# Kernel tuning notes

Hardware: AMD Instinct MI355X
Metric: run time of the kernel (lower is better)

Reference implementation:

```python
import jax, jax.numpy as jnp
import numpy as np
import math

DIM = 768
NUM_HEADS = 12
HEAD_DIM = DIM // NUM_HEADS


def setup_inputs() -> dict:
    key = jax.random.key(0)
    k_x, k_q, k_k, k_v = jax.random.split(key, 4)
    s = 1.0 / math.sqrt(DIM)
    return {
        "x": jax.random.normal(k_x, (2, 2048, DIM), dtype=jnp.float32),
        "Wq": jax.random.normal(k_q, (DIM, DIM), dtype=jnp.float32) * s,
        "Wk": jax.random.normal(k_k, (DIM, DIM), dtype=jnp.float32) * s,
        "Wv": jax.random.normal(k_v, (DIM, DIM), dtype=jnp.float32) * s,
    }


def reference(x, Wq, Wk, Wv):
    b, n, _ = x.shape
    # nn.Linear(dim, dim, bias=False): y = x @ W.T
    def split_heads(y):
        return y.reshape(b, n, NUM_HEADS, HEAD_DIM).transpose(0, 2, 1, 3)  # b h n d
    Q = split_heads(x @ Wq.T)
    K = split_heads(x @ Wk.T)
    V = split_heads(x @ Wv.T)
    scores = jnp.einsum('bhqd,bhkd->bhqk', Q, K)
    # FAITHFUL to source: softmax over the HEADS axis (dim=1), then scale by 1/sqrt(dim)
    attn = jax.nn.softmax(scores, axis=1) / math.sqrt(DIM)
    out = jnp.einsum('bhqk,bhkd->bhqd', attn, V)
    out = out.transpose(0, 2, 1, 3).reshape(b, n, DIM)  # b n (h d)
    return out  # to_out is Identity (project_out=False)
```

## Files before the change

### kernel.cpp

```cpp
#include <hip/hip_runtime.h>

#define DIM 768
#define NHEADS 12
#define HDIM 64
#define BATCH 2
#define SEQ 2048
#define ROWS (BATCH*SEQ)
#define KSPLIT 4

typedef __attribute__((ext_vector_type(8))) _Float16 f16x8;
typedef __attribute__((ext_vector_type(4))) _Float16 f16x4;
typedef __attribute__((ext_vector_type(2))) _Float16 f16x2;
typedef __attribute__((ext_vector_type(4))) float    f32x4;

__device__ __forceinline__ void dma16(const _Float16* g, _Float16* l) {
    __builtin_amdgcn_global_load_lds(
        (const __attribute__((address_space(1))) unsigned int*)g,
        (__attribute__((address_space(3))) unsigned int*)l, 16, 0, 0);
}


__global__ __launch_bounds__(256) void cvt_all(
    const float* __restrict__ x,  const float* __restrict__ wq,
    const float* __restrict__ wk, const float* __restrict__ wv,
    _Float16* __restrict__ xf,  _Float16* __restrict__ wqf,
    _Float16* __restrict__ wkf, _Float16* __restrict__ wvf)
{
    const int lane = threadIdx.x & 63;
    const int wid  = (blockIdx.x * 256 + threadIdx.x) >> 6;
    const float* src; _Float16* dst; int t;
    if (wid < 6144)      { src = x;  dst = xf;  t = wid;        }
    else if (wid < 7296) { src = wq; dst = wqf; t = wid - 6144; }
    else if (wid < 8448) { src = wk; dst = wkf; t = wid - 7296; }
    else                 { src = wv; dst = wvf; t = wid - 8448; }
    const int c = lane & 15, quad = lane >> 4;
    const int mt = t / 24, kt = t % 24;
    const float* p = src + (size_t)(mt*16 + c) * 768 + kt*32 + quad*8;
    float4 v0 = *(const float4*)p;
    float4 v1 = *(const float4*)(p + 4);
    f16x8 o;
    o[0]=(_Float16)v0.x; o[1]=(_Float16)v0.y; o[2]=(_Float16)v0.z; o[3]=(_Float16)v0.w;
    o[4]=(_Float16)v1.x; o[5]=(_Float16)v1.y; o[6]=(_Float16)v1.z; o[7]=(_Float16)v1.w;
    *reinterpret_cast<f16x8*>(dst + ((size_t)t * 64 + lane) * 8) = o;
}

__global__ __launch_bounds__(256) void gemm3(
    const _Float16* __restrict__ xf, const _Float16* __restrict__ wqkf,
    const _Float16* __restrict__ wvf,
    _Float16* __restrict__ Qf, _Float16* __restrict__ Kf, _Float16* __restrict__ Vkt)
{
    __shared__ _Float16 Ab[2][8*512];
    __shared__ _Float16 Bb[2][8*512];
    const int tid = threadIdx.x, lane = tid & 63, w = tid >> 6;
    const int c = lane & 15, quad = lane >> 4;

    const _Float16 *Af, *Bf;
    int mt0, nt0, mode;
    if ((int)blockIdx.x < 384) {
        int mt = blockIdx.x / 12, nt = blockIdx.x % 12;
        Af = xf; Bf = wqkf; mt0 = mt*8; nt0 = nt*8; mode = 0;
    } else {
        int v = blockIdx.x - 384;
        int mt = v / 32, nt = v % 32;
        Af = wvf; Bf = xf; mt0 = mt*8; nt0 = nt*8; mode = 1;
    }

    auto stage = [&](int kt, int buf) {
#pragma unroll
        for (int u = 0; u < 4; ++u) {
            const int cc = w*4 + u;
            const _Float16* s = (cc < 8) ? Af + ((size_t)(mt0+cc)*24 + kt)*512
                                         : Bf + ((size_t)(nt0+cc-8)*24 + kt)*512;
            _Float16* d = (cc < 8) ? &Ab[buf][cc*512] : &Bb[buf][(cc-8)*512];
            dma16(s + lane*8, d);
        }
    };

    stage(0, 0);
    __syncthreads();

    f32x4 acc[4][4] = {};
    for (int kt = 0; kt < 24; ++kt) {
        const int cur = kt & 1;
        if (kt < 23) stage(kt+1, cur^1);
        f16x8 a[4], b[4];
#pragma unroll
        for (int i = 0; i < 4; ++i)
            a[i] = *(const f16x8*)(&Ab[cur][((w>>1)*4 + i)*512] + lane*8);
#pragma unroll
        for (int j = 0; j < 4; ++j)
            b[j] = *(const f16x8*)(&Bb[cur][((w&1)*4 + j)*512] + lane*8);
#pragma unroll
        for (int i = 0; i < 4; ++i)
#pragma unroll
            for (int j = 0; j < 4; ++j)
                acc[i][j] = __builtin_amdgcn_mfma_f32_16x16x32_f16(a[i], b[j], acc[i][j], 0,0,0);
        __syncthreads();
    }

    _Float16* L = &Ab[0][0] + w*1280;
#pragma unroll
    for (int i2 = 0; i2 < 2; ++i2)
#pragma unroll
        for (int j2 = 0; j2 < 2; ++j2) {
#pragma unroll
            for (int ii = 0; ii < 2; ++ii)
#pragma unroll
                for (int jj = 0; jj < 2; ++jj)
#pragma unroll
                    for (int r = 0; r < 4; ++r)
                        L[(ii*16 + quad*4 + r)*40 + jj*16 + c] =
                            (_Float16)acc[i2*2+ii][j2*2+jj][r];
#pragma unroll
            for (int ii = 0; ii < 2; ++ii) {
                const int mtg = mt0 + (w>>1)*4 + i2*2 + ii;
                if (mode == 0) {
                    f16x8 v = *(const f16x8*)(L + (ii*16 + c)*40 + quad*8);
                    const int nt32 = (nt0 + (w&1)*4)/2 + j2;
                    _Float16* dst = (nt32 < 24)
                        ? Qf + ((size_t)(mtg*24 + nt32)*64 + lane)*8
                        : Kf + ((size_t)(mtg*24 + nt32 - 24)*64 + lane)*8;
                    *(f16x8*)dst = v;
                } else {
#pragma unroll
                    for (int jj = 0; jj < 2; ++jj) {
                        f16x4 v4 = *(const f16x4*)(L + (ii*16 + c)*40 + jj*16 + quad*4);
                        const int kcu = nt0 + (w&1)*4 + j2*2 + jj;
                        *(f16x4*)(Vkt + ((size_t)kcu*48 + mtg)*256 + lane*4) = v4;
                    }
                }
            }
        }
}

__global__ __launch_bounds__(1024) __attribute__((amdgpu_waves_per_eu(4)))
void attn_kernel(
    const _Float16* __restrict__ Qf, const _Float16* __restrict__ Kf,
    const _Float16* __restrict__ Vkt,
    float* __restrict__ out,
    _Float16* __restrict__ part)
{
    __shared__ __attribute__((aligned(16))) _Float16 Kb[24*512];
    __shared__ __attribute__((aligned(16))) float    Ps[16][16][20];
    __shared__ __attribute__((aligned(16))) _Float16 Pl[4][12][16][20];
    const int tid = threadIdx.x, lane = tid & 63, w = tid >> 6;
    const int c = lane & 15, quad = lane >> 4;
    const int qi = w >> 2, g = w & 3;

    const int bid = blockIdx.x;
    const int qb = bid & 31;
    const int ks = (bid >> 5) & 3;
    const int b  = bid >> 7;
    const int qrow0 = b*SEQ + qb*64;
    const int qt16  = (qrow0 >> 4) + qi;
    const int kb16  = (b*SEQ + ks*(SEQ/KSPLIT)) >> 4;

    f16x8 qreg[6];
#pragma unroll
    for (int u = 0; u < 6; ++u)
        qreg[u] = *(const f16x8*)(Qf + ((size_t)(qt16*24 + g*6 + u)*64 + lane)*8);

    const _Float16* Vb0 = Vkt + ((size_t)kb16*48 + g)*256 + lane*4;

    if (w < 12) {
#pragma unroll
        for (int u = 0; u < 2; ++u)
            dma16(Kf + ((size_t)kb16*24 + w*2 + u)*512 + lane*8, &Kb[(w*2+u)*512]);
    }
    __syncthreads();

    f32x4 o_acc[12] = {};
    f16x4 vv[12];
    f32x4 e3[3];

    for (int t = 0; t < 32; ++t) {
#pragma unroll
        for (int hh = 0; hh < 3; ++hh) {
            f16x8 ka = *(const f16x8*)(&Kb[(g*6 + hh*2    )*512] + lane*8);
            f16x8 k2 = *(const f16x8*)(&Kb[(g*6 + hh*2 + 1)*512] + lane*8);
            f32x4 a = {};
            a = __builtin_amdgcn_mfma_f32_16x16x32_f16(ka, qreg[hh*2],   a, 0,0,0);
            a = __builtin_amdgcn_mfma_f32_16x16x32_f16(k2, qreg[hh*2+1], a, 0,0,0);
            f32x4 ee;
#pragma unroll
            for (int r = 0; r < 4; ++r) ee[r] = __expf(a[r]);
            e3[hh] = ee;
        }
        {
            f32x4 ps;
#pragma unroll
            for (int r = 0; r < 4; ++r) ps[r] = e3[0][r] + e3[1][r] + e3[2][r];
            *(f32x4*)&Ps[qi*4+g][c][quad*4] = ps;
        }
        if (t > 0) {
#pragma unroll
            for (int h = 6; h < 12; ++h)
                vv[h] = *(const f16x4*)(Vb0 + ((size_t)(t-1)*48 + h*4)*256);
#pragma unroll
            for (int h = 0; h < 12; ++h) {
                f16x4 pf = *(const f16x4*)&Pl[qi][h][c][quad*4];
                o_acc[h] = __builtin_amdgcn_mfma_f32_16x16x16f16(vv[h], pf, o_acc[h], 0,0,0);
            }
        }
        __syncthreads();
        if (w < 12 && t < 31) {
#pragma unroll
            for (int u = 0; u < 2; ++u)
                dma16(Kf + ((size_t)(kb16+t+1)*24 + w*2 + u)*512 + lane*8,
                      &Kb[(w*2+u)*512]);
        }
        {
            f32x4 s0 = *(const f32x4*)&Ps[qi*4+0][c][quad*4];
            f32x4 s1 = *(const f32x4*)&Ps[qi*4+1][c][quad*4];
            f32x4 s2 = *(const f32x4*)&Ps[qi*4+2][c][quad*4];
            f32x4 s3 = *(const f32x4*)&Ps[qi*4+3][c][quad*4];
            f32x4 inv;
#pragma unroll
            for (int r = 0; r < 4; ++r)
                inv[r] = 1.0f / ((s0[r]+s1[r]+s2[r]+s3[r]) * 27.712812921102035f);
#pragma unroll
            for (int hh = 0; hh < 3; ++hh) {
                f16x4 pw;
#pragma unroll
                for (int r = 0; r < 4; ++r) pw[r] = (_Float16)(e3[hh][r]*inv[r]);
                *(f16x4*)&Pl[qi][g*3+hh][c][quad*4] = pw;
            }
        }
#pragma unroll
        for (int h = 0; h < 6; ++h)
            vv[h] = *(const f16x4*)(Vb0 + ((size_t)t*48 + h*4)*256);
        __syncthreads();
    }
#pragma unroll
    for (int h = 6; h < 12; ++h)
        vv[h] = *(const f16x4*)(Vb0 + ((size_t)31*48 + h*4)*256);
#pragma unroll
    for (int h = 0; h < 12; ++h) {
        f16x4 pf = *(const f16x4*)&Pl[qi][h][c][quad*4];
        o_acc[h] = __builtin_amdgcn_mfma_f32_16x16x16f16(vv[h], pf, o_acc[h], 0,0,0);
    }

    if (ks == 0) {
#pragma unroll
        for (int h = 0; h < 12; ++h)
            *(f32x4*)(out + (size_t)(qrow0 + qi*16 + c)*DIM + h*64 + g*16 + quad*4)
                = o_acc[h];
    } else {
        _Float16* dst = part + (size_t)(ks - 1) * ROWS * DIM;
#pragma unroll
        for (int h = 0; h < 12; ++h) {
            f16x4 v;
#pragma unroll
            for (int r = 0; r < 4; ++r) v[r] = (_Float16)o_acc[h][r];
            *(f16x4*)(dst + (size_t)(qrow0 + qi*16 + c)*DIM + h*64 + g*16 + quad*4) = v;
        }
    }
}

__global__ __launch_bounds__(256) void reduce_add4(
    float* __restrict__ out, const _Float16* __restrict__ part, int n4)
{
    int i = blockIdx.x * 256 + threadIdx.x;
    if (i >= n4) return;
    float4 o = reinterpret_cast<float4*>(out)[i];
    const size_t N = (size_t)ROWS * DIM;
#pragma unroll
    for (int p = 0; p < 3; ++p) {
        f16x4 v = reinterpret_cast<const f16x4*>(part + p * N)[i];
        o.x += (float)v[0]; o.y += (float)v[1]; o.z += (float)v[2]; o.w += (float)v[3];
    }
    reinterpret_cast<float4*>(out)[i] = o;
}

extern "C" void kernel_launch(void* const* d_in, const int* in_sizes, int n_in,
                              void* d_out, int out_size, void* d_ws, size_t ws_size,
                              hipStream_t stream)
{
    const float* x  = (const float*)d_in[0];
    const float* Wq = (const float*)d_in[1];
    const float* Wk = (const float*)d_in[2];
    const float* Wv = (const float*)d_in[3];

    _Float16* ws  = (_Float16*)d_ws;
    const size_t XS = (size_t)ROWS * DIM;
    const size_t WS = (size_t)DIM * DIM;
    _Float16* xf   = ws;
    _Float16* wqf  = xf  + XS;
    _Float16* wkf  = wqf + WS;
    _Float16* wvf  = wkf + WS;
    _Float16* Qf   = wvf + WS;
    _Float16* Kf   = Qf  + XS;
    _Float16* Vkt  = Kf  + XS;
    _Float16* part = Vkt + XS;

    cvt_all<<<2400, 256, 0, stream>>>(x, Wq, Wk, Wv, xf, wqf, wkf, wvf);
    gemm3<<<576, 256, 0, stream>>>(xf, wqf, wvf, Qf, Kf, Vkt);
    attn_kernel<<<BATCH * KSPLIT * 32, 1024, 0, stream>>>(
        Qf, Kf, Vkt, (float*)d_out, part);
    reduce_add4<<<(int)(XS/4 + 255)/256, 256, 0, stream>>>(
        (float*)d_out, part, (int)(XS/4));
}
```

Before: 188.6 us.

## Prefetch K tiles through registers and use LDS-only barriers

Replaces the global_load_lds DMA of K tiles with register prefetch two steps ahead, storing into LDS after the barrier. __syncthreads is replaced with s_waitcnt lgkmcnt(0) plus s_barrier, so outstanding global loads (V and K prefetch) no longer block at barriers. All 12 V fragments are now loaded at the end of each step rather than split across two phases, and the Ps scratch layout changes to a padded flat layout meant to reduce LDS bank conflicts. This raises register pressure and relies on the compiler inserting vmcnt waits correctly before the prefetched registers are used.

Result: slower. 230.7 us (+22.3%).

```diff
diff --git a/kernel.cpp b/kernel.cpp
--- a/kernel.cpp
+++ b/kernel.cpp
@@ -17,6 +17,10 @@
     __builtin_amdgcn_global_load_lds(
         (const __attribute__((address_space(1))) unsigned int*)g,
         (__attribute__((address_space(3))) unsigned int*)l, 16, 0, 0);
+}
+
+__device__ __forceinline__ void barrier_lgkm() {
+    asm volatile("s_waitcnt lgkmcnt(0)\n\ts_barrier" ::: "memory");
 }
 
 
@@ -141,7 +145,7 @@
     _Float16* __restrict__ part)
 {
     __shared__ __attribute__((aligned(16))) _Float16 Kb[24*512];
-    __shared__ __attribute__((aligned(16))) float    Ps[16][16][20];
+    __shared__ __attribute__((aligned(16))) float    Ps[16][336];
     __shared__ __attribute__((aligned(16))) _Float16 Pl[4][12][16][20];
     const int tid = threadIdx.x, lane = tid & 63, w = tid >> 6;
     const int c = lane & 15, quad = lane >> 4;
@@ -154,6 +158,7 @@
     const int qrow0 = b*SEQ + qb*64;
     const int qt16  = (qrow0 >> 4) + qi;
     const int kb16  = (b*SEQ + ks*(SEQ/KSPLIT)) >> 4;
+    const int psoff = quad*84 + c*4;
 
     f16x8 qreg[6];
 #pragma unroll
@@ -162,12 +167,17 @@
 
     const _Float16* Vb0 = Vkt + ((size_t)kb16*48 + g)*256 + lane*4;
 
+    f16x8 kreg0, kreg1;
     if (w < 12) {
-#pragma unroll
-        for (int u = 0; u < 2; ++u)
-            dma16(Kf + ((size_t)kb16*24 + w*2 + u)*512 + lane*8, &Kb[(w*2+u)*512]);
-    }
-    __syncthreads();
+        const _Float16* kp = Kf + ((size_t)kb16*24 + w*2)*512 + lane*8;
+        kreg0 = *(const f16x8*)(kp);
+        kreg1 = *(const f16x8*)(kp + 512);
+        *(f16x8*)(&Kb[(w*2+0)*512] + lane*8) = kreg0;
+        *(f16x8*)(&Kb[(w*2+1)*512] + lane*8) = kreg1;
+        kreg0 = *(const f16x8*)(kp + 24*512);
+        kreg1 = *(const f16x8*)(kp + 24*512 + 512);
+    }
+    barrier_lgkm();
 
     f32x4 o_acc[12] = {};
     f16x4 vv[12];
@@ -190,30 +200,30 @@
             f32x4 ps;
 #pragma unroll
             for (int r = 0; r < 4; ++r) ps[r] = e3[0][r] + e3[1][r] + e3[2][r];
-            *(f32x4*)&Ps[qi*4+g][c][quad*4] = ps;
+            *(f32x4*)&Ps[qi*4+g][psoff] = ps;
         }
         if (t > 0) {
-#pragma unroll
-            for (int h = 6; h < 12; ++h)
-                vv[h] = *(const f16x4*)(Vb0 + ((size_t)(t-1)*48 + h*4)*256);
 #pragma unroll
             for (int h = 0; h < 12; ++h) {
                 f16x4 pf = *(const f16x4*)&Pl[qi][h][c][quad*4];
                 o_acc[h] = __builtin_amdgcn_mfma_f32_16x16x16f16(vv[h], pf, o_acc[h], 0,0,0);
             }
         }
-        __syncthreads();
+        barrier_lgkm();
         if (w < 12 && t < 31) {
-#pragma unroll
-            for (int u = 0; u < 2; ++u)
-                dma16(Kf + ((size_t)(kb16+t+1)*24 + w*2 + u)*512 + lane*8,
-                      &Kb[(w*2+u)*512]);
+            *(f16x8*)(&Kb[(w*2+0)*512] + lane*8) = kreg0;
+            *(f16x8*)(&Kb[(w*2+1)*512] + lane*8) = kreg1;
+            if (t < 30) {
+                const _Float16* kp = Kf + ((size_t)(kb16+t+2)*24 + w*2)*512 + lane*8;
+                kreg0 = *(const f16x8*)(kp);
+                kreg1 = *(const f16x8*)(kp + 512);
+            }
         }
         {
-            f32x4 s0 = *(const f32x4*)&Ps[qi*4+0][c][quad*4];
-            f32x4 s1 = *(const f32x4*)&Ps[qi*4+1][c][quad*4];
-            f32x4 s2 = *(const f32x4*)&Ps[qi*4+2][c][quad*4];
-            f32x4 s3 = *(const f32x4*)&Ps[qi*4+3][c][quad*4];
+            f32x4 s0 = *(const f32x4*)&Ps[qi*4+0][psoff];
+            f32x4 s1 = *(const f32x4*)&Ps[qi*4+1][psoff];
+            f32x4 s2 = *(const f32x4*)&Ps[qi*4+2][psoff];
+            f32x4 s3 = *(const f32x4*)&Ps[qi*4+3][psoff];
             f32x4 inv;
 #pragma unroll
             for (int r = 0; r < 4; ++r)
@@ -227,13 +237,10 @@
             }
         }
 #pragma unroll
-        for (int h = 0; h < 6; ++h)
+        for (int h = 0; h < 12; ++h)
             vv[h] = *(const f16x4*)(Vb0 + ((size_t)t*48 + h*4)*256);
-        __syncthreads();
-    }
-#pragma unroll
-    for (int h = 6; h < 12; ++h)
-        vv[h] = *(const f16x4*)(Vb0 + ((size_t)31*48 + h*4)*256);
+        barrier_lgkm();
+    }
 #pragma unroll
     for (int h = 0; h < 12; ++h) {
         f16x4 pf = *(const f16x4*)&Pl[qi][h][c][quad*4];
```

## Halve attention block size, fold log2e into Wq, use exp2 and fast reciprocal

Applied to the files above, without the earlier changes.

Shrinks the attention block from 1024 to 512 threads, with 32 query rows per block and twice as many blocks. Every wave now issues three K DMA loads, where before only 12 of 16 waves issued two each. Wq is pre-scaled by log2(e) during conversion so the softmax can use the hardware exp2 instead of expf, and the normaliser uses a fast rcp instead of a divide. The Ps LDS layout is padded differently to reduce bank conflicts, and all 12 V loads are issued together after the barrier. Together these aim to raise occupancy and cut transcendental cost, but K is loaded twice as often overall and precision drops slightly.

Result: no change. 188.2 us (-0.2%).

```diff
diff --git a/kernel.cpp b/kernel.cpp
--- a/kernel.cpp
+++ b/kernel.cpp
@@ -29,8 +29,9 @@
     const int lane = threadIdx.x & 63;
     const int wid  = (blockIdx.x * 256 + threadIdx.x) >> 6;
     const float* src; _Float16* dst; int t;
+    float sc = 1.0f;
     if (wid < 6144)      { src = x;  dst = xf;  t = wid;        }
-    else if (wid < 7296) { src = wq; dst = wqf; t = wid - 6144; }
+    else if (wid < 7296) { src = wq; dst = wqf; t = wid - 6144; sc = 1.4426950408889634f; }
     else if (wid < 8448) { src = wk; dst = wkf; t = wid - 7296; }
     else                 { src = wv; dst = wvf; t = wid - 8448; }
     const int c = lane & 15, quad = lane >> 4;
@@ -39,8 +40,8 @@
     float4 v0 = *(const float4*)p;
     float4 v1 = *(const float4*)(p + 4);
     f16x8 o;
-    o[0]=(_Float16)v0.x; o[1]=(_Float16)v0.y; o[2]=(_Float16)v0.z; o[3]=(_Float16)v0.w;
-    o[4]=(_Float16)v1.x; o[5]=(_Float16)v1.y; o[6]=(_Float16)v1.z; o[7]=(_Float16)v1.w;
+    o[0]=(_Float16)(v0.x*sc); o[1]=(_Float16)(v0.y*sc); o[2]=(_Float16)(v0.z*sc); o[3]=(_Float16)(v0.w*sc);
+    o[4]=(_Float16)(v1.x*sc); o[5]=(_Float16)(v1.y*sc); o[6]=(_Float16)(v1.z*sc); o[7]=(_Float16)(v1.w*sc);
     *reinterpret_cast<f16x8*>(dst + ((size_t)t * 64 + lane) * 8) = o;
 }
 
@@ -133,7 +134,7 @@
         }
 }
 
-__global__ __launch_bounds__(1024) __attribute__((amdgpu_waves_per_eu(4)))
+__global__ __launch_bounds__(512) __attribute__((amdgpu_waves_per_eu(4)))
 void attn_kernel(
     const _Float16* __restrict__ Qf, const _Float16* __restrict__ Kf,
     const _Float16* __restrict__ Vkt,
@@ -141,19 +142,20 @@
     _Float16* __restrict__ part)
 {
     __shared__ __attribute__((aligned(16))) _Float16 Kb[24*512];
-    __shared__ __attribute__((aligned(16))) float    Ps[16][16][20];
-    __shared__ __attribute__((aligned(16))) _Float16 Pl[4][12][16][20];
+    __shared__ __attribute__((aligned(16))) float    Ps[8][336];
+    __shared__ __attribute__((aligned(16))) _Float16 Pl[2][12][16][20];
     const int tid = threadIdx.x, lane = tid & 63, w = tid >> 6;
     const int c = lane & 15, quad = lane >> 4;
     const int qi = w >> 2, g = w & 3;
 
     const int bid = blockIdx.x;
-    const int qb = bid & 31;
-    const int ks = (bid >> 5) & 3;
-    const int b  = bid >> 7;
-    const int qrow0 = b*SEQ + qb*64;
+    const int qb = bid & 63;
+    const int ks = (bid >> 6) & 3;
+    const int b  = bid >> 8;
+    const int qrow0 = b*SEQ + qb*32;
     const int qt16  = (qrow0 >> 4) + qi;
     const int kb16  = (b*SEQ + ks*(SEQ/KSPLIT)) >> 4;
+    const int psoff = quad*84 + c*4;
 
     f16x8 qreg[6];
 #pragma unroll
@@ -162,11 +164,9 @@
 
     const _Float16* Vb0 = Vkt + ((size_t)kb16*48 + g)*256 + lane*4;
 
-    if (w < 12) {
-#pragma unroll
-        for (int u = 0; u < 2; ++u)
-            dma16(Kf + ((size_t)kb16*24 + w*2 + u)*512 + lane*8, &Kb[(w*2+u)*512]);
-    }
+#pragma unroll
+    for (int u = 0; u < 3; ++u)
+        dma16(Kf + ((size_t)kb16*24 + w*3 + u)*512 + lane*8, &Kb[(w*3+u)*512]);
     __syncthreads();
 
     f32x4 o_acc[12] = {};
@@ -183,19 +183,16 @@
             a = __builtin_amdgcn_mfma_f32_16x16x32_f16(k2, qreg[hh*2+1], a, 0,0,0);
             f32x4 ee;
 #pragma unroll
-            for (int r = 0; r < 4; ++r) ee[r] = __expf(a[r]);
+            for (int r = 0; r < 4; ++r) ee[r] = __builtin_amdgcn_exp2f(a[r]);
             e3[hh] = ee;
         }
         {
             f32x4 ps;
 #pragma unroll
             for (int r = 0; r < 4; ++r) ps[r] = e3[0][r] + e3[1][r] + e3[2][r];
-            *(f32x4*)&Ps[qi*4+g][c][quad*4] = ps;
+            *(f32x4*)&Ps[qi*4+g][psoff] = ps;
         }
         if (t > 0) {
-#pragma unroll
-            for (int h = 6; h < 12; ++h)
-                vv[h] = *(const f16x4*)(Vb0 + ((size_t)(t-1)*48 + h*4)*256);
 #pragma unroll
             for (int h = 0; h < 12; ++h) {
                 f16x4 pf = *(const f16x4*)&Pl[qi][h][c][quad*4];
@@ -203,21 +200,22 @@
             }
         }
         __syncthreads();
-        if (w < 12 && t < 31) {
-#pragma unroll
-            for (int u = 0; u < 2; ++u)
-                dma16(Kf + ((size_t)(kb16+t+1)*24 + w*2 + u)*512 + lane*8,
-                      &Kb[(w*2+u)*512]);
+        if (t < 31) {
+#pragma unroll
+            for (int u = 0; u < 3; ++u)
+                dma16(Kf + ((size_t)(kb16+t+1)*24 + w*3 + u)*512 + lane*8,
+                      &Kb[(w*3+u)*512]);
         }
         {
-            f32x4 s0 = *(const f32x4*)&Ps[qi*4+0][c][quad*4];
-            f32x4 s1 = *(const f32x4*)&Ps[qi*4+1][c][quad*4];
-            f32x4 s2 = *(const f32x4*)&Ps[qi*4+2][c][quad*4];
-            f32x4 s3 = *(const f32x4*)&Ps[qi*4+3][c][quad*4];
+            f32x4 s0 = *(const f32x4*)&Ps[qi*4+0][psoff];
+            f32x4 s1 = *(const f32x4*)&Ps[qi*4+1][psoff];
+            f32x4 s2 = *(const f32x4*)&Ps[qi*4+2][psoff];
+            f32x4 s3 = *(const f32x4*)&Ps[qi*4+3][psoff];
             f32x4 inv;
 #pragma unroll
             for (int r = 0; r < 4; ++r)
-                inv[r] = 1.0f / ((s0[r]+s1[r]+s2[r]+s3[r]) * 27.712812921102035f);
+                inv[r] = __builtin_amdgcn_rcpf(
+                    (s0[r]+s1[r]+s2[r]+s3[r]) * 27.712812921102035f);
 #pragma unroll
             for (int hh = 0; hh < 3; ++hh) {
                 f16x4 pw;
@@ -227,13 +225,10 @@
             }
         }
 #pragma unroll
-        for (int h = 0; h < 6; ++h)
+        for (int h = 0; h < 12; ++h)
             vv[h] = *(const f16x4*)(Vb0 + ((size_t)t*48 + h*4)*256);
         __syncthreads();
     }
-#pragma unroll
-    for (int h = 6; h < 12; ++h)
-        vv[h] = *(const f16x4*)(Vb0 + ((size_t)31*48 + h*4)*256);
 #pragma unroll
     for (int h = 0; h < 12; ++h) {
         f16x4 pf = *(const f16x4*)&Pl[qi][h][c][quad*4];
@@ -295,7 +290,7 @@
 
     cvt_all<<<2400, 256, 0, stream>>>(x, Wq, Wk, Wv, xf, wqf, wkf, wvf);
     gemm3<<<576, 256, 0, stream>>>(xf, wqf, wvf, Qf, Kf, Vkt);
-    attn_kernel<<<BATCH * KSPLIT * 32, 1024, 0, stream>>>(
+    attn_kernel<<<BATCH * KSPLIT * 64, 512, 0, stream>>>(
         Qf, Kf, Vkt, (float*)d_out, part);
     reduce_add4<<<(int)(XS/4 + 255)/256, 256, 0, stream>>>(
         (float*)d_out, part, (int)(XS/4));
```
